# Kernel tuning notes

Hardware: AMD Instinct MI355X
Metric: run time of the kernel (lower is better)

Reference implementation:

```python
import jax, jax.numpy as jnp
import numpy as np

N_TF, N_GENES, W, FANIN, B = 1024, 20000, 4, 16, 128
M = N_GENES * W  # middle width = 80000


def _build_edges(rng):
    # layer 1: each of the M per-gene nodes draws FANIN random TF inputs
    out1 = np.repeat(np.arange(M, dtype=np.int32), FANIN)
    in1 = rng.integers(0, N_TF, size=M * FANIN).astype(np.int32)
    in1[-1] = N_TF - 1  # ensure full input dim is touched
    # layer 2: dense WxW block per gene (node i of gene g sees all W nodes of gene g)
    out2 = np.repeat(np.arange(M, dtype=np.int32), W)
    gene = np.arange(M, dtype=np.int32) // W
    in2 = (gene[:, None] * W + np.arange(W, dtype=np.int32)[None, :]).reshape(-1)
    # layer 3: each gene output sums its W nodes
    out3 = np.repeat(np.arange(N_GENES, dtype=np.int32), W)
    in3 = np.arange(M, dtype=np.int32)
    return out1, in1, out2, in2, out3, in3


def setup_inputs() -> dict:
    key = jax.random.key(0)
    ks = jax.random.split(key, 7)
    rng = np.random.default_rng(0)
    out1, in1, out2, in2, out3, in3 = _build_edges(rng)
    scale1 = 1.0 / np.sqrt(FANIN)
    scale2 = 1.0 / np.sqrt(W)
    return {
        "features": jax.random.normal(ks[0], (B, N_TF), jnp.float32),
        "w1": jax.random.normal(ks[1], (out1.shape[0],), jnp.float32) * scale1,
        "b1": jax.random.normal(ks[2], (M,), jnp.float32) * 0.01,
        "w2": jax.random.normal(ks[3], (out2.shape[0],), jnp.float32) * scale2,
        "b2": jax.random.normal(ks[4], (M,), jnp.float32) * 0.01,
        "w3": jax.random.normal(ks[5], (out3.shape[0],), jnp.float32) * scale2,
        "b3": jax.random.normal(ks[6], (N_GENES,), jnp.float32) * 0.01,
        "out1": jnp.asarray(out1), "in1": jnp.asarray(in1),
        "out2": jnp.asarray(out2), "in2": jnp.asarray(in2),
        "out3": jnp.asarray(out3), "in3": jnp.asarray(in3),
    }


def _sparse_linear(x, w, b, out_idx, in_idx):
    # x: [B, n_in]; per-edge gather-multiply-scatter, y[b, o] = sum_e w_e * x[b, in_e] + b_o
    contrib = x.T[in_idx] * w[:, None]                      # [nnz, B]
    y = jax.ops.segment_sum(contrib, out_idx, num_segments=b.shape[0])  # [n_out, B]
    return y.T + b


def reference(features, w1, b1, w2, b2, w3, b3, out1, in1, out2, in2, out3, in3):
    h = jnp.tanh(_sparse_linear(features, w1, b1, out1, in1))
    h = jnp.tanh(_sparse_linear(h, w2, b2, out2, in2))
    return _sparse_linear(h, w3, b3, out3, in3)  # [B, N_GENES]
```

## Files before the change

kernel.cpp:

```cpp
#include <hip/hip_runtime.h>
#include <hip/hip_bf16.h>

#define N_TF    1024
#define N_GENES 20000
#define WW      4
#define FANIN   16
#define BATCH   128

__device__ __forceinline__ float fast_tanh(float x) {
    float t = __expf(2.0f * x);
    return 1.0f - 2.0f * __builtin_amdgcn_rcpf(t + 1.0f);
}

__global__ __launch_bounds__(256) void transpose_kernel(
    const float* __restrict__ in, float* __restrict__ out)
{
    __shared__ float tile[32][33];
    const int bx = blockIdx.x;
    const int by = blockIdx.y;
    const int tx = threadIdx.x;
    const int ty = threadIdx.y;
#pragma unroll
    for (int k = 0; k < 32; k += 8)
        tile[ty + k][tx] = in[(by * 32 + ty + k) * N_TF + bx * 32 + tx];
    __syncthreads();
#pragma unroll
    for (int k = 0; k < 32; k += 8)
        out[(bx * 32 + ty + k) * BATCH + by * 32 + tx] = tile[tx][ty + k];
}

constexpr int GENES_PER_BLOCK = 16;
constexpr int GENES_PER_WAVE  = 4;
constexpr int YPAD            = 130;

__global__ __launch_bounds__(256) void fused_kernel(
    const float* __restrict__ xT,
    const float* __restrict__ w1,
    const float* __restrict__ b1,
    const int*   __restrict__ in1,
    const float* __restrict__ w2,
    const float* __restrict__ b2,
    const float* __restrict__ w3,
    const float* __restrict__ b3,
    float*       __restrict__ out)
{
    __shared__ float ytile[GENES_PER_BLOCK * YPAD];

    const int tid  = threadIdx.x;
    const int wid  = __builtin_amdgcn_readfirstlane(tid >> 6);
    const int lane = tid & 63;
    const int g_base = blockIdx.x * GENES_PER_BLOCK + wid * GENES_PER_WAVE;
    const float2* __restrict__ xT2 = (const float2*)xT;

    for (int gi = 0; gi < GENES_PER_WAVE; ++gi) {
        const int g = g_base + gi;

        float2 h1[WW];
#pragma unroll
        for (int i = 0; i < WW; ++i) {
            const int o = g * WW + i;
            const int ebase = o * FANIN;
            float ax = 0.0f, ay = 0.0f;
#pragma unroll
            for (int j = 0; j < FANIN; ++j) {
                const float w   = w1[ebase + j];
                const int   idx = in1[ebase + j];
                const float2 xv = xT2[idx * (BATCH / 2) + lane];
                ax += w * xv.x;
                ay += w * xv.y;
            }
            const float bb = b1[o];
            h1[i].x = fast_tanh(ax + bb);
            h1[i].y = fast_tanh(ay + bb);
        }

        float2 h2[WW];
#pragma unroll
        for (int i = 0; i < WW; ++i) {
            const int o = g * WW + i;
            float sx = b2[o], sy = sx;
#pragma unroll
            for (int k = 0; k < WW; ++k) {
                const float w = w2[o * WW + k];
                sx += w * h1[k].x;
                sy += w * h1[k].y;
            }
            h2[i].x = fast_tanh(sx);
            h2[i].y = fast_tanh(sy);
        }

        float yx = b3[g], yy = yx;
#pragma unroll
        for (int i = 0; i < WW; ++i) {
            const float w = w3[g * WW + i];
            yx += w * h2[i].x;
            yy += w * h2[i].y;
        }

        const int gl = wid * GENES_PER_WAVE + gi;
        ytile[gl * YPAD + 2 * lane]     = yx;
        ytile[gl * YPAD + 2 * lane + 1] = yy;
    }

    __syncthreads();

    const int g0 = blockIdx.x * GENES_PER_BLOCK;
#pragma unroll
    for (int it = 0; it < (GENES_PER_BLOCK * BATCH) / 256; ++it) {
        const int idx = it * 256 + tid;
        const int gl  = idx & (GENES_PER_BLOCK - 1);
        const int b   = idx >> 4;
        out[b * N_GENES + g0 + gl] = ytile[gl * YPAD + b];
    }
}

extern "C" void kernel_launch(void* const* d_in, const int* in_sizes, int n_in,
                              void* d_out, int out_size, void* d_ws, size_t ws_size,
                              hipStream_t stream)
{
    const float* features = (const float*)d_in[0];
    const float* w1 = (const float*)d_in[1];
    const float* b1 = (const float*)d_in[2];
    const float* w2 = (const float*)d_in[3];
    const float* b2 = (const float*)d_in[4];
    const float* w3 = (const float*)d_in[5];
    const float* b3 = (const float*)d_in[6];
    const int*   in1 = (const int*)d_in[8];
    float* out = (float*)d_out;

    float* xT = (float*)d_ws;

    hipLaunchKernelGGL(transpose_kernel, dim3(32, 4), dim3(32, 8), 0, stream,
                       features, xT);
    hipLaunchKernelGGL(fused_kernel, dim3(N_GENES / GENES_PER_BLOCK), dim3(256), 0, stream,
                       xT, w1, b1, in1, w2, b2, w3, b3, out);
}
```

Measured before the change: 134.8 us.

## Use fp16 transposed features with half2 FMA and one gene per wave

The transpose now converts features to fp16, and layer-1 gathers plus accumulation run in packed half2 FMA with the edge index made wave-uniform through readfirstlane. The fused kernel changes from 256 threads doing four genes per wave to 512 threads doing one gene per wave, and it uses float4 weight loads and a paired tanh that shares one reciprocal. The aim is to halve gather bandwidth and cut instruction count. Accumulating 16 products in fp16 reduces accuracy and may exceed tolerance.

```diff
diff --git a/kernel.cpp b/kernel.cpp
--- a/kernel.cpp
+++ b/kernel.cpp
@@ -1,19 +1,30 @@
 #include <hip/hip_runtime.h>
-#include <hip/hip_bf16.h>
+#include <hip/hip_fp16.h>
 
 #define N_TF    1024
 #define N_GENES 20000
 #define WW      4
 #define FANIN   16
 #define BATCH   128
+#define NNZ1    (N_GENES * WW * FANIN)
 
-__device__ __forceinline__ float fast_tanh(float x) {
-    float t = __expf(2.0f * x);
-    return 1.0f - 2.0f * __builtin_amdgcn_rcpf(t + 1.0f);
+#define GENES_PER_BLOCK 8
+#define NTHREADS        512
+#define NBLK            (N_GENES / GENES_PER_BLOCK)
+#define YROW            (BATCH + 2)
+
+__device__ __forceinline__ float2 fast_tanh2(float a, float b) {
+    const float ta = __expf(2.0f * a);
+    const float tb = __expf(2.0f * b);
+    const float da = ta + 1.0f;
+    const float db = tb + 1.0f;
+    const float r  = __builtin_amdgcn_rcpf(da * db);
+    return make_float2(fmaf(-2.0f * db, r, 1.0f),
+                       fmaf(-2.0f * da, r, 1.0f));
 }
 
-__global__ __launch_bounds__(256) void transpose_kernel(
-    const float* __restrict__ in, float* __restrict__ out)
+__global__ __launch_bounds__(256) void transpose_cvt_kernel(
+    const float* __restrict__ in, __half* __restrict__ out)
 {
     __shared__ float tile[32][33];
     const int bx = blockIdx.x;
@@ -24,93 +35,90 @@
     for (int k = 0; k < 32; k += 8)
         tile[ty + k][tx] = in[(by * 32 + ty + k) * N_TF + bx * 32 + tx];
     __syncthreads();
+    const int b = by * 32 + tx;
 #pragma unroll
-    for (int k = 0; k < 32; k += 8)
-        out[(bx * 32 + ty + k) * BATCH + by * 32 + tx] = tile[tx][ty + k];
+    for (int k = 0; k < 32; k += 8) {
+        const int tf = bx * 32 + ty + k;
+        out[tf * BATCH + b] = __float2half(tile[tx][ty + k]);
+    }
 }
 
-constexpr int GENES_PER_BLOCK = 16;
-constexpr int GENES_PER_WAVE  = 4;
-constexpr int YPAD            = 130;
-
-__global__ __launch_bounds__(256) void fused_kernel(
-    const float* __restrict__ xT,
-    const float* __restrict__ w1,
-    const float* __restrict__ b1,
-    const int*   __restrict__ in1,
-    const float* __restrict__ w2,
-    const float* __restrict__ b2,
-    const float* __restrict__ w3,
-    const float* __restrict__ b3,
-    float*       __restrict__ out)
+__global__ __launch_bounds__(NTHREADS, 8) void fused_kernel(
+    const __half* __restrict__ xh,
+    const float*  __restrict__ w1,
+    const float*  __restrict__ b1,
+    const int*    __restrict__ in1,
+    const float*  __restrict__ w2,
+    const float*  __restrict__ b2,
+    const float*  __restrict__ w3,
+    const float*  __restrict__ b3,
+    float*        __restrict__ out)
 {
-    __shared__ float ytile[GENES_PER_BLOCK * YPAD];
+    __shared__ float yt[GENES_PER_BLOCK * YROW];
 
     const int tid  = threadIdx.x;
     const int wid  = __builtin_amdgcn_readfirstlane(tid >> 6);
     const int lane = tid & 63;
-    const int g_base = blockIdx.x * GENES_PER_BLOCK + wid * GENES_PER_WAVE;
-    const float2* __restrict__ xT2 = (const float2*)xT;
+    const int g    = blockIdx.x * GENES_PER_BLOCK + wid;
 
-    for (int gi = 0; gi < GENES_PER_WAVE; ++gi) {
-        const int g = g_base + gi;
+    const int eb = g * (WW * FANIN);
+    __half2 acc[WW];
+    const __half2 hz = __float2half2_rn(0.0f);
+#pragma unroll
+    for (int i = 0; i < WW; ++i) acc[i] = hz;
 
-        float2 h1[WW];
+#pragma unroll
+    for (int j = 0; j < FANIN; ++j) {
 #pragma unroll
         for (int i = 0; i < WW; ++i) {
-            const int o = g * WW + i;
-            const int ebase = o * FANIN;
-            float ax = 0.0f, ay = 0.0f;
+            const int e   = eb + i * FANIN + j;
+            const int idx = __builtin_amdgcn_readfirstlane(in1[e]);
+            const float wf = w1[e];
+            const __half2 wv = __float2half2_rn(wf);
+            const __half2 xv = *((const __half2*)(xh + idx * BATCH) + lane);
+            acc[i] = __hfma2(wv, xv, acc[i]);
+        }
+    }
+
+    float2 h1[WW];
 #pragma unroll
-            for (int j = 0; j < FANIN; ++j) {
-                const float w   = w1[ebase + j];
-                const int   idx = in1[ebase + j];
-                const float2 xv = xT2[idx * (BATCH / 2) + lane];
-                ax += w * xv.x;
-                ay += w * xv.y;
-            }
-            const float bb = b1[o];
-            h1[i].x = fast_tanh(ax + bb);
-            h1[i].y = fast_tanh(ay + bb);
-        }
+    for (int i = 0; i < WW; ++i) {
+        const float  bb = b1[g * WW + i];
+        const float2 af = __half22float2(acc[i]);
+        h1[i] = fast_tanh2(af.x + bb, af.y + bb);
+    }
 
-        float2 h2[WW];
+    float2 h2[WW];
 #pragma unroll
-        for (int i = 0; i < WW; ++i) {
-            const int o = g * WW + i;
-            float sx = b2[o], sy = sx;
-#pragma unroll
-            for (int k = 0; k < WW; ++k) {
-                const float w = w2[o * WW + k];
-                sx += w * h1[k].x;
-                sy += w * h1[k].y;
-            }
-            h2[i].x = fast_tanh(sx);
-            h2[i].y = fast_tanh(sy);
-        }
+    for (int i = 0; i < WW; ++i) {
+        const float4 w  = *(const float4*)(w2 + g * 16 + i * 4);
+        const float  bb = b2[g * WW + i];
+        const float sx = bb + w.x * h1[0].x + w.y * h1[1].x
+                            + w.z * h1[2].x + w.w * h1[3].x;
+        const float sy = bb + w.x * h1[0].y + w.y * h1[1].y
+                            + w.z * h1[2].y + w.w * h1[3].y;
+        h2[i] = fast_tanh2(sx, sy);
+    }
 
-        float yx = b3[g], yy = yx;
-#pragma unroll
-        for (int i = 0; i < WW; ++i) {
-            const float w = w3[g * WW + i];
-            yx += w * h2[i].x;
-            yy += w * h2[i].y;
-        }
+    const float4 wv = *(const float4*)(w3 + g * 4);
+    const float  bv = b3[g];
+    const float yx = bv + wv.x * h2[0].x + wv.y * h2[1].x
+                        + wv.z * h2[2].x + wv.w * h2[3].x;
+    const float yy = bv + wv.x * h2[0].y + wv.y * h2[1].y
+                        + wv.z * h2[2].y + wv.w * h2[3].y;
 
-        const int gl = wid * GENES_PER_WAVE + gi;
-        ytile[gl * YPAD + 2 * lane]     = yx;
-        ytile[gl * YPAD + 2 * lane + 1] = yy;
-    }
+    float2* ytw = (float2*)(yt + wid * YROW);
+    ytw[lane] = make_float2(yx, yy);
 
     __syncthreads();
 
     const int g0 = blockIdx.x * GENES_PER_BLOCK;
 #pragma unroll
-    for (int it = 0; it < (GENES_PER_BLOCK * BATCH) / 256; ++it) {
-        const int idx = it * 256 + tid;
-        const int gl  = idx & (GENES_PER_BLOCK - 1);
-        const int b   = idx >> 4;
-        out[b * N_GENES + g0 + gl] = ytile[gl * YPAD + b];
+    for (int it = 0; it < (BATCH * GENES_PER_BLOCK) / NTHREADS; ++it) {
+        const int idx = it * NTHREADS + tid;
+        const int gq  = idx & (GENES_PER_BLOCK - 1);
+        const int b   = idx >> 3;
+        out[b * N_GENES + g0 + gq] = yt[gq * YROW + b];
     }
 }
 
@@ -128,10 +136,10 @@
     const int*   in1 = (const int*)d_in[8];
     float* out = (float*)d_out;
 
-    float* xT = (float*)d_ws;
+    __half* xh = (__half*)d_ws;
 
-    hipLaunchKernelGGL(transpose_kernel, dim3(32, 4), dim3(32, 8), 0, stream,
-                       features, xT);
-    hipLaunchKernelGGL(fused_kernel, dim3(N_GENES / GENES_PER_BLOCK), dim3(256), 0, stream,
-                       xT, w1, b1, in1, w2, b2, w3, b3, out);
+    hipLaunchKernelGGL(transpose_cvt_kernel, dim3(32, 4), dim3(32, 8), 0, stream,
+                       features, xh);
+    hipLaunchKernelGGL(fused_kernel, dim3(NBLK), dim3(NTHREADS), 0, stream,
+                       xh, w1, b1, in1, w2, b2, w3, b3, out);
 }
```

New measurement: 116.4 us. 13.7% less time.
